# Kernel tuning notes

Hardware: AMD Instinct MI355X
Metric: run time of the kernel (lower is better)

Reference implementation:

```python
import jax, jax.numpy as jnp
import numpy as np

K = 512   # cardinality of each hidden source
O = 8     # n_out per party
NS = 3    # number of sources (triangle network)


def setup_inputs() -> dict:
    key = jax.random.key(0)
    k1, k2 = jax.random.split(key)
    n_pred = NS * K + 3 * K * K * O
    y_pred = jax.random.uniform(k1, (1, n_pred), dtype=jnp.float32)
    y_true = jax.random.uniform(k2, (O ** 3,), dtype=jnp.float32)
    y_true = y_true / jnp.sum(y_true)  # a proper target distribution
    return {"y_pred": y_pred, "y_true": y_true}


def _distribution(y_pred):
    # sources block: [NS, K] source probability tables
    srcs = y_pred[0, :NS * K].reshape(NS, K)
    pf = y_pred[0, NS * K:]
    sz = K * K * O
    # party response tensors, indexed by the two source symbols the party sees
    A = pf[:sz].reshape(K, K, O)          # A sees (beta, gamma) -> (j, k)
    B = pf[sz:2 * sz].reshape(K, K, O)    # B sees (gamma, alpha) -> (k, i)
    C = pf[2 * sz:].reshape(K, K, O)      # C sees (alpha, beta) -> (i, j)
    Pa, Pb, Pc = srcs[0], srcs[1], srcs[2]
    # prob[x,y,z] = sum_{i,j,k} Pa[i] Pb[j] Pc[k] A[j,k,x] B[k,i,y] C[i,j,z]
    Aw = A * Pb[:, None, None] * Pc[None, :, None]   # [j,k,x]
    Bw = B * Pa[None, :, None]                        # [k,i,y]
    T = jnp.einsum('jkx,kiy->ijxy', Aw, Bw)           # contract k; [K,K,O,O]
    probs = jnp.einsum('ijxy,ijz->xyz', T, C)         # contract i,j; [O,O,O]
    return probs.reshape(-1)


def reference(y_pred, y_true):
    probs = _distribution(y_pred)
    log_p = jnp.log(jnp.clip(probs, 1e-10, 1.0))
    d = jnp.sum(y_true * (jnp.log(y_true + 1e-10) - log_p))
    return (d, probs)
```

## Files before the change

kernel.cpp:

```cpp
#include <hip/hip_runtime.h>
#include <hip/hip_bf16.h>
#include <stdint.h>

#define KD 512
#define OD 8
#define SZ (KD*KD*OD)
#define PLANE (KD*KD)

typedef short v8s __attribute__((ext_vector_type(8)));
typedef float v4f __attribute__((ext_vector_type(4)));

#define GLOBAL_AS __attribute__((address_space(1)))
#define LDS_AS __attribute__((address_space(3)))

static __device__ __forceinline__ unsigned short f2bf(float f) {
    union { float f; unsigned int u; } v; v.f = f;
    unsigned int u = v.u;
    unsigned int r = u + 0x7FFF + ((u >> 16) & 1);
    return (unsigned short)(r >> 16);
}

static __device__ __forceinline__ void async16(const unsigned short* g, unsigned short* l) {
    __builtin_amdgcn_global_load_lds((const GLOBAL_AS void*)g, (LDS_AS void*)l, 16, 0, 0);
}

static __device__ __forceinline__ v8s lds_frag(const unsigned short* base, int row, int colb) {
    return *(const v8s*)((const char*)base + row * 128 + (colb ^ ((row & 7) << 4)));
}

__global__ __launch_bounds__(256) void pack_kernel(const float* __restrict__ yp,
                                                   unsigned short* __restrict__ Wbf,
                                                   unsigned short* __restrict__ Xbf,
                                                   float* __restrict__ probs_acc) {
    __shared__ unsigned short lds[8 * 32 * 32];
    const float* Pa = yp;
    const float* Pb = yp + KD;
    const float* Pc = yp + 2 * KD;
    const float* A  = yp + 3 * KD;
    const float* B  = A + SZ;
    const int b = blockIdx.x;
    const int t = threadIdx.x;

    if (b == 0) { probs_acc[t] = 0.0f; probs_acc[t + 256] = 0.0f; }

    if (b < 256) {
        #pragma unroll
        for (int jj = 0; jj < 2; ++jj) {
            const int j = b * 2 + jj;
            const float pb = Pb[j];
            const int k0 = 2 * t;
            const float4* src = (const float4*)(A + ((size_t)j * KD + k0) * 8);
            float av[16];
            ((float4*)av)[0] = src[0];
            ((float4*)av)[1] = src[1];
            ((float4*)av)[2] = src[2];
            ((float4*)av)[3] = src[3];
            const float s0 = pb * Pc[k0];
            const float s1 = pb * Pc[k0 + 1];
            #pragma unroll
            for (int x = 0; x < 8; ++x) {
                ushort2 w;
                w.x = f2bf(av[x] * s0);
                w.y = f2bf(av[8 + x] * s1);
                *(ushort2*)(Wbf + (size_t)x * PLANE + (size_t)j * KD + k0) = w;
            }
        }
    } else {
        const int tb = b - 256;
        const int k0 = (tb / 16) * 32;
        const int i0 = (tb % 16) * 32;
        char* ldsb = (char*)lds;
        #pragma unroll
        for (int p = 0; p < 4; ++p) {
            const int idx = t + p * 256;
            const int dk = idx >> 5;
            const int di = idx & 31;
            const float pa = Pa[i0 + di];
            const float4* src = (const float4*)(B + ((size_t)(k0 + dk) * KD + (i0 + di)) * 8);
            float bv[8];
            ((float4*)bv)[0] = src[0];
            ((float4*)bv)[1] = src[1];
            const int swz = (di & 7) << 4;
            #pragma unroll
            for (int y = 0; y < 8; ++y)
                *(unsigned short*)(ldsb + (y * 32 + di) * 64 + ((dk * 2) ^ swz)) =
                    f2bf(bv[y] * pa);
        }
        __syncthreads();
        #pragma unroll
        for (int p = 0; p < 4; ++p) {
            const int c = t + p * 256;
            const int y = c >> 7;
            const int rem = c & 127;
            const int di = rem >> 2;
            const int dk8 = (rem & 3) * 8;
            uint4 v = *(const uint4*)(ldsb + (y * 32 + di) * 64 + ((dk8 * 2) ^ ((di & 7) << 4)));
            *(uint4*)(Xbf + (size_t)y * PLANE + (size_t)(i0 + di) * KD + (k0 + dk8)) = v;
        }
    }
}

__global__ __launch_bounds__(256, 3) void gemm_kernel(const float* __restrict__ yp,
                                                      const unsigned short* __restrict__ Wbf,
                                                      const unsigned short* __restrict__ Xbf,
                                                      float* __restrict__ probs_acc) {
    __shared__ unsigned short S[4][64 * 64];
    __shared__ float red[4][32];

    const int bid = blockIdx.x;
    const int xcd = bid & 7;
    const int local = bid >> 3;
    const int tl = local >> 4;
    const int group = local & 15;
    const int i_t = ((xcd >> 1) << 1) | (tl >> 2);
    const int j_t = ((xcd & 1) << 2) | (tl & 3);
    const int i0 = i_t * 64, j0 = j_t * 64;
    const int x0 = (group >> 2) * 2, y0 = (group & 3) * 2;

    const int t = threadIdx.x;
    const int w = t >> 6;
    const int l = t & 63;
    const int wm = w >> 1, wn = w & 1;
    const int lm = l & 15, quad = l >> 4;
    const int srow = l >> 3;
    const int scol = ((l & 7) ^ srow) * 8;

    const unsigned short* gsrc;
    if (w < 2) gsrc = Xbf + (size_t)(y0 + w) * PLANE + (size_t)i0 * KD;
    else       gsrc = Wbf + (size_t)(x0 + (w - 2)) * PLANE + (size_t)j0 * KD;
    const unsigned short* gthr = gsrc + (size_t)srow * KD + scol;

    v4f acc[2][2][2][2];
    #pragma unroll
    for (int a = 0; a < 2; ++a)
      #pragma unroll
      for (int bb = 0; bb < 2; ++bb)
        #pragma unroll
        for (int c = 0; c < 2; ++c)
          #pragma unroll
          for (int d = 0; d < 2; ++d)
            acc[a][bb][c][d] = (v4f){0.f, 0.f, 0.f, 0.f};

    for (int kt = 0; kt < 8; ++kt) {
        const int kbase = kt * 64;
        #pragma unroll
        for (int q = 0; q < 8; ++q)
            async16(gthr + (size_t)(q * 8) * KD + kbase, &S[w][q * 512]);
        __syncthreads();

        #pragma unroll
        for (int kk = 0; kk < 2; ++kk) {
            const int colb = kk * 64 + quad * 16;
            v8s aF[2][2], bF[2][2];
            #pragma unroll
            for (int dy = 0; dy < 2; ++dy)
                #pragma unroll
                for (int mt = 0; mt < 2; ++mt)
                    aF[dy][mt] = lds_frag(&S[dy][0], wm * 32 + mt * 16 + lm, colb);
            #pragma unroll
            for (int dx = 0; dx < 2; ++dx)
                #pragma unroll
                for (int nt = 0; nt < 2; ++nt)
                    bF[dx][nt] = lds_frag(&S[2 + dx][0], wn * 32 + nt * 16 + lm, colb);
            #pragma unroll
            for (int dy = 0; dy < 2; ++dy)
                #pragma unroll
                for (int dx = 0; dx < 2; ++dx)
                    #pragma unroll
                    for (int mt = 0; mt < 2; ++mt)
                        #pragma unroll
                        for (int nt = 0; nt < 2; ++nt)
                            acc[dy][dx][mt][nt] = __builtin_amdgcn_mfma_f32_16x16x32_bf16(
                                aF[dy][mt], bF[dx][nt], acc[dy][dx][mt][nt], 0, 0, 0);
        }
        __syncthreads();
    }

    const float* Cp = yp + 3 * KD + 2 * (size_t)SZ;
    float zacc[2][2][8];
    #pragma unroll
    for (int dy = 0; dy < 2; ++dy)
      #pragma unroll
      for (int dx = 0; dx < 2; ++dx)
        #pragma unroll
        for (int z = 0; z < 8; ++z) zacc[dy][dx][z] = 0.f;

    #pragma unroll
    for (int mt = 0; mt < 2; ++mt) {
        #pragma unroll
        for (int nt = 0; nt < 2; ++nt) {
            #pragma unroll
            for (int r = 0; r < 4; ++r) {
                const int gi = i0 + wm * 32 + mt * 16 + quad * 4 + r;
                const int gj = j0 + wn * 32 + nt * 16 + lm;
                const float4* cp = (const float4*)(Cp + ((size_t)gi * KD + gj) * 8);
                const float4 c0 = cp[0], c1 = cp[1];
                #pragma unroll
                for (int dy = 0; dy < 2; ++dy) {
                    #pragma unroll
                    for (int dx = 0; dx < 2; ++dx) {
                        const float tv = acc[dy][dx][mt][nt][r];
                        zacc[dy][dx][0] += tv * c0.x; zacc[dy][dx][1] += tv * c0.y;
                        zacc[dy][dx][2] += tv * c0.z; zacc[dy][dx][3] += tv * c0.w;
                        zacc[dy][dx][4] += tv * c1.x; zacc[dy][dx][5] += tv * c1.y;
                        zacc[dy][dx][6] += tv * c1.z; zacc[dy][dx][7] += tv * c1.w;
                    }
                }
            }
        }
    }
    #pragma unroll
    for (int dy = 0; dy < 2; ++dy)
      #pragma unroll
      for (int dx = 0; dx < 2; ++dx)
        #pragma unroll
        for (int z = 0; z < 8; ++z) {
            float v = zacc[dy][dx][z];
            for (int off = 32; off > 0; off >>= 1)
                v += __shfl_xor(v, off, 64);
            zacc[dy][dx][z] = v;
        }
    if (l == 0) {
        #pragma unroll
        for (int dy = 0; dy < 2; ++dy)
          #pragma unroll
          for (int dx = 0; dx < 2; ++dx)
            #pragma unroll
            for (int z = 0; z < 8; ++z)
                red[w][(dy * 2 + dx) * 8 + z] = zacc[dy][dx][z];
    }
    __syncthreads();
    if (t < 32) {
        const float s = red[0][t] + red[1][t] + red[2][t] + red[3][t];
        const int p = t >> 3;
        const int dy = p >> 1, dx = p & 1, z = t & 7;
        atomicAdd(&probs_acc[((x0 + dx) * 8 + (y0 + dy)) * 8 + z], s);
    }
}

__global__ __launch_bounds__(512) void finalize_kernel(const float* __restrict__ probs_acc,
                                                       const float* __restrict__ y_true,
                                                       float* __restrict__ out) {
    __shared__ float red[8];
    const int t = threadIdx.x;
    const float p = probs_acc[t];
    out[1 + t] = p;
    const float ytv = y_true[t];
    const float pc = fminf(fmaxf(p, 1e-10f), 1.0f);
    float term = ytv * (logf(ytv + 1e-10f) - logf(pc));
    for (int off = 32; off > 0; off >>= 1)
        term += __shfl_xor(term, off, 64);
    if ((t & 63) == 0) red[t >> 6] = term;
    __syncthreads();
    if (t == 0) {
        float s = 0.f;
        #pragma unroll
        for (int i = 0; i < 8; ++i) s += red[i];
        out[0] = s;
    }
}

extern "C" void kernel_launch(void* const* d_in, const int* in_sizes, int n_in,
                              void* d_out, int out_size, void* d_ws, size_t ws_size,
                              hipStream_t stream) {
    const float* yp = (const float*)d_in[0];
    const float* yt = (const float*)d_in[1];
    float* out = (float*)d_out;

    unsigned short* Wbf = (unsigned short*)d_ws;
    unsigned short* Xbf = Wbf + (size_t)8 * PLANE;
    float* probs_acc = (float*)(Xbf + (size_t)8 * PLANE);

    pack_kernel<<<512, 256, 0, stream>>>(yp, Wbf, Xbf, probs_acc);
    gemm_kernel<<<1024, 256, 0, stream>>>(yp, Wbf, Xbf, probs_acc);
    finalize_kernel<<<1, 512, 0, stream>>>(probs_acc, yt, out);
}
```

Baseline: 101.6 us.

## Load GEMM fragments directly from global memory instead of staging through LDS

Removes the LDS staging buffer and the async global-to-LDS copies in the GEMM kernel. Each lane now loads its MFMA fragments straight from global/L2 with 16-byte vector loads, unrolled by 4 over 16 k-steps. The change also drops the block barriers, raises the occupancy hint to 4 blocks, and adds s_setprio around the MFMA bursts. The aim is to cut barrier and LDS overhead, at the cost of redundant global loads across waves (A/B fragments reused by two waves each) and more reliance on cache hit rates.

```diff
diff --git a/kernel.cpp b/kernel.cpp
--- a/kernel.cpp
+++ b/kernel.cpp
@@ -9,23 +9,12 @@
 
 typedef short v8s __attribute__((ext_vector_type(8)));
 typedef float v4f __attribute__((ext_vector_type(4)));
-
-#define GLOBAL_AS __attribute__((address_space(1)))
-#define LDS_AS __attribute__((address_space(3)))
 
 static __device__ __forceinline__ unsigned short f2bf(float f) {
     union { float f; unsigned int u; } v; v.f = f;
     unsigned int u = v.u;
     unsigned int r = u + 0x7FFF + ((u >> 16) & 1);
     return (unsigned short)(r >> 16);
-}
-
-static __device__ __forceinline__ void async16(const unsigned short* g, unsigned short* l) {
-    __builtin_amdgcn_global_load_lds((const GLOBAL_AS void*)g, (LDS_AS void*)l, 16, 0, 0);
-}
-
-static __device__ __forceinline__ v8s lds_frag(const unsigned short* base, int row, int colb) {
-    return *(const v8s*)((const char*)base + row * 128 + (colb ^ ((row & 7) << 4)));
 }
 
 __global__ __launch_bounds__(256) void pack_kernel(const float* __restrict__ yp,
@@ -100,11 +89,10 @@
     }
 }
 
-__global__ __launch_bounds__(256, 3) void gemm_kernel(const float* __restrict__ yp,
+__global__ __launch_bounds__(256, 4) void gemm_kernel(const float* __restrict__ yp,
                                                       const unsigned short* __restrict__ Wbf,
                                                       const unsigned short* __restrict__ Xbf,
                                                       float* __restrict__ probs_acc) {
-    __shared__ unsigned short S[4][64 * 64];
     __shared__ float red[4][32];
 
     const int bid = blockIdx.x;
@@ -122,13 +110,21 @@
     const int l = t & 63;
     const int wm = w >> 1, wn = w & 1;
     const int lm = l & 15, quad = l >> 4;
-    const int srow = l >> 3;
-    const int scol = ((l & 7) ^ srow) * 8;
-
-    const unsigned short* gsrc;
-    if (w < 2) gsrc = Xbf + (size_t)(y0 + w) * PLANE + (size_t)i0 * KD;
-    else       gsrc = Wbf + (size_t)(x0 + (w - 2)) * PLANE + (size_t)j0 * KD;
-    const unsigned short* gthr = gsrc + (size_t)srow * KD + scol;
+
+    const unsigned short* aP[2][2];
+    const unsigned short* bP[2][2];
+    #pragma unroll
+    for (int dy = 0; dy < 2; ++dy)
+        #pragma unroll
+        for (int mt = 0; mt < 2; ++mt)
+            aP[dy][mt] = Xbf + (size_t)(y0 + dy) * PLANE
+                       + (size_t)(i0 + wm * 32 + mt * 16 + lm) * KD + quad * 8;
+    #pragma unroll
+    for (int dx = 0; dx < 2; ++dx)
+        #pragma unroll
+        for (int nt = 0; nt < 2; ++nt)
+            bP[dx][nt] = Wbf + (size_t)(x0 + dx) * PLANE
+                       + (size_t)(j0 + wn * 32 + nt * 16 + lm) * KD + quad * 8;
 
     v4f acc[2][2][2][2];
     #pragma unroll
@@ -141,39 +137,32 @@
           for (int d = 0; d < 2; ++d)
             acc[a][bb][c][d] = (v4f){0.f, 0.f, 0.f, 0.f};
 
-    for (int kt = 0; kt < 8; ++kt) {
-        const int kbase = kt * 64;
-        #pragma unroll
-        for (int q = 0; q < 8; ++q)
-            async16(gthr + (size_t)(q * 8) * KD + kbase, &S[w][q * 512]);
-        __syncthreads();
-
-        #pragma unroll
-        for (int kk = 0; kk < 2; ++kk) {
-            const int colb = kk * 64 + quad * 16;
-            v8s aF[2][2], bF[2][2];
-            #pragma unroll
-            for (int dy = 0; dy < 2; ++dy)
+    #pragma unroll 4
+    for (int kt = 0; kt < 16; ++kt) {
+        const int kof = kt * 32;
+        v8s aF[2][2], bF[2][2];
+        #pragma unroll
+        for (int dy = 0; dy < 2; ++dy)
+            #pragma unroll
+            for (int mt = 0; mt < 2; ++mt)
+                aF[dy][mt] = *(const v8s*)(aP[dy][mt] + kof);
+        #pragma unroll
+        for (int dx = 0; dx < 2; ++dx)
+            #pragma unroll
+            for (int nt = 0; nt < 2; ++nt)
+                bF[dx][nt] = *(const v8s*)(bP[dx][nt] + kof);
+        __builtin_amdgcn_s_setprio(1);
+        #pragma unroll
+        for (int dy = 0; dy < 2; ++dy)
+            #pragma unroll
+            for (int dx = 0; dx < 2; ++dx)
                 #pragma unroll
                 for (int mt = 0; mt < 2; ++mt)
-                    aF[dy][mt] = lds_frag(&S[dy][0], wm * 32 + mt * 16 + lm, colb);
-            #pragma unroll
-            for (int dx = 0; dx < 2; ++dx)
-                #pragma unroll
-                for (int nt = 0; nt < 2; ++nt)
-                    bF[dx][nt] = lds_frag(&S[2 + dx][0], wn * 32 + nt * 16 + lm, colb);
-            #pragma unroll
-            for (int dy = 0; dy < 2; ++dy)
-                #pragma unroll
-                for (int dx = 0; dx < 2; ++dx)
                     #pragma unroll
-                    for (int mt = 0; mt < 2; ++mt)
-                        #pragma unroll
-                        for (int nt = 0; nt < 2; ++nt)
-                            acc[dy][dx][mt][nt] = __builtin_amdgcn_mfma_f32_16x16x32_bf16(
-                                aF[dy][mt], bF[dx][nt], acc[dy][dx][mt][nt], 0, 0, 0);
-        }
-        __syncthreads();
+                    for (int nt = 0; nt < 2; ++nt)
+                        acc[dy][dx][mt][nt] = __builtin_amdgcn_mfma_f32_16x16x32_bf16(
+                            aF[dy][mt], bF[dx][nt], acc[dy][dx][mt][nt], 0, 0, 0);
+        __builtin_amdgcn_s_setprio(0);
     }
 
     const float* Cp = yp + 3 * KD + 2 * (size_t)SZ;
```

Measured after the change: 138.4 us. +36.2%, slower.
